# Kernel optimization log

Measured on AMD Instinct MI355X. Metric: run time of the kernel, lower is better.

Reference implementation:

```python
import jax, jax.numpy as jnp
import numpy as np

B, TQ, TK, D = 8, 2048, 2048, 1024


def setup_inputs() -> dict:
    key = jax.random.key(0)
    ks = jax.random.split(key, 9)
    s = 1.0 / np.sqrt(D)
    return {
        "query": jax.random.normal(ks[0], (B, TQ, D), jnp.float32),
        "keys": jax.random.normal(ks[1], (B, TK, D), jnp.float32),
        "Wq": jax.random.normal(ks[2], (D, D), jnp.float32) * s,
        "bq": jax.random.normal(ks[3], (D,), jnp.float32) * 0.01,
        "Wk": jax.random.normal(ks[4], (D, D), jnp.float32) * s,
        "bk": jax.random.normal(ks[5], (D,), jnp.float32) * 0.01,
        "Wv": jax.random.normal(ks[6], (D, D), jnp.float32) * s,
        "bv": jax.random.normal(ks[7], (D,), jnp.float32) * 0.01,
        "mask": jax.random.randint(ks[8], (B, TQ, TK), 0, 2, jnp.int32),
    }


def reference(query, keys, Wq, bq, Wk, bk, Wv, bv, mask):
    # Projections (torch Linear math; weights stored as [in, out])
    q = query @ Wq + bq            # [B, TQ, D]
    k = keys @ Wk + bk             # [B, TK, D]
    v = keys @ Wv + bv             # proj_values=True -> [B, TK, D]
    scale = 1.0 / jnp.sqrt(jnp.asarray(D, q.dtype))
    scores = jnp.einsum("bqd,bkd->bqk", q, k) * scale  # [B, TQ, TK]
    scores = jnp.where(mask == 0, jnp.asarray(-1e9, scores.dtype), scores)
    alphas = jax.nn.softmax(scores, axis=-1)
    context = jnp.einsum("bqk,bkd->bqd", alphas, v)    # [B, TQ, D]
    return context
```

## Files before the change

kernel.cpp:

```cpp
#include <hip/hip_runtime.h>
#include <hip/hip_bf16.h>

#define BB 8
#define TQn 2048
#define TKn 2048
#define DDn 1024

typedef float f32x4 __attribute__((ext_vector_type(4)));
typedef short bf16x8 __attribute__((ext_vector_type(8)));

__device__ __forceinline__ void async16(const void* g, void* l) {
    __builtin_amdgcn_global_load_lds(
        (const __attribute__((address_space(1))) void*)g,
        (__attribute__((address_space(3))) void*)l, 16, 0, 0);
}

__global__ __launch_bounds__(256) void prep_k(
    float* __restrict__ rowsum, float* __restrict__ biasqk,
    const float* __restrict__ bq, const float* __restrict__ bk) {
    int i = blockIdx.x * 256 + threadIdx.x;
    if (i < BB * TQn) rowsum[i] = 0.0f;
    if (i < DDn) biasqk[i] = bq[i];
    else if (i < 2 * DDn) biasqk[i] = bk[i - DDn];
}

__global__ __launch_bounds__(256) void cast2_k(
    const float* __restrict__ q, const float* __restrict__ k,
    __hip_bfloat16* __restrict__ xq, __hip_bfloat16* __restrict__ xk, size_t n8) {
    const float* in = blockIdx.y ? k : q;
    __hip_bfloat16* out = blockIdx.y ? xk : xq;
    size_t i = (size_t)blockIdx.x * blockDim.x + threadIdx.x;
    size_t stride = (size_t)gridDim.x * blockDim.x;
    for (; i < n8; i += stride) {
        const float4* p = (const float4*)in + i * 2;
        float4 a = p[0], b = p[1];
        union { __hip_bfloat16 h[8]; int4 qd; } u;
        u.h[0] = __float2bfloat16(a.x); u.h[1] = __float2bfloat16(a.y);
        u.h[2] = __float2bfloat16(a.z); u.h[3] = __float2bfloat16(a.w);
        u.h[4] = __float2bfloat16(b.x); u.h[5] = __float2bfloat16(b.y);
        u.h[6] = __float2bfloat16(b.z); u.h[7] = __float2bfloat16(b.w);
        ((int4*)out)[i] = u.qd;
    }
}

__global__ __launch_bounds__(256) void transpose3_k(
    const float* __restrict__ Wq, const float* __restrict__ Wk,
    const float* __restrict__ Wv, __hip_bfloat16* __restrict__ oq,
    __hip_bfloat16* __restrict__ ok, __hip_bfloat16* __restrict__ ov) {
    const float* in = blockIdx.z == 0 ? Wq : (blockIdx.z == 1 ? Wk : Wv);
    __hip_bfloat16* out = blockIdx.z == 0 ? oq : (blockIdx.z == 1 ? ok : ov);
    __shared__ float tile[32][33];
    int c0 = blockIdx.x * 32, r0 = blockIdx.y * 32;
    int tx = threadIdx.x, ty = threadIdx.y;
    #pragma unroll
    for (int i = 0; i < 32; i += 8)
        tile[ty + i][tx] = in[(size_t)(r0 + ty + i) * DDn + c0 + tx];
    __syncthreads();
    #pragma unroll
    for (int i = 0; i < 32; i += 8)
        out[(size_t)(c0 + ty + i) * DDn + r0 + tx] = __float2bfloat16(tile[tx][ty + i]);
}

#define M_PROJ_QK 0
#define M_PROJ_V  1
#define M_SCORES  2
#define M_CTX     3

#define STG(Pg, Psl, U, T, H) do { \
    const __hip_bfloat16* _g = Pg + (size_t)(T) * 64 + (H) * 32; \
    char* _l = Psl + (U) * 16384 + w * 2048; \
    async16(_g, _l); \
    async16(_g + 16 * Kd, _l + 1024); \
} while (0)

#define PHASE(U, S, STAGE_STMT, WAIT_STMT) do { \
    if ((S) == 0) { \
        _Pragma("unroll") \
        for (int m = 0; m < 8; m++) \
            af[m] = *(const bf16x8*)(Asl + (U) * 16384 + a_off + m * 1024); \
    } \
    bf[0] = *(const bf16x8*)(Bsl + (U) * 16384 + b_off + (S) * 2048); \
    bf[1] = *(const bf16x8*)(Bsl + (U) * 16384 + b_off + (S) * 2048 + 1024); \
    STAGE_STMT; \
    WAIT_STMT; \
    __builtin_amdgcn_sched_barrier(0); \
    __builtin_amdgcn_s_barrier(); \
    __builtin_amdgcn_s_setprio(1); \
    _Pragma("unroll") \
    for (int m = 0; m < 8; m++) { \
        acc[m][(S)*2]     = __builtin_amdgcn_mfma_f32_16x16x32_bf16(af[m], bf[0], acc[m][(S)*2], 0, 0, 0); \
        acc[m][(S)*2 + 1] = __builtin_amdgcn_mfma_f32_16x16x32_bf16(af[m], bf[1], acc[m][(S)*2 + 1], 0, 0, 0); \
    } \
    __builtin_amdgcn_s_setprio(0); \
    __builtin_amdgcn_sched_barrier(0); \
    __builtin_amdgcn_s_barrier(); \
} while (0)

template <int MODE>
__global__ __launch_bounds__(512, 2) void gemm256_k(
    const __hip_bfloat16* __restrict__ A, const __hip_bfloat16* __restrict__ B,
    void* __restrict__ Cout, const float* __restrict__ bias,
    const int* __restrict__ mask, float* __restrict__ rowsum,
    int K, long sA, long sB, long sC, float scale, int ldc) {
    __shared__ char smem[131072];
    char* Asl = smem;
    char* Bsl = smem + 65536;

    const int tid = threadIdx.x;
    const int lane = tid & 63;
    const int w = tid >> 6;
    const int wr = w >> 2, wc = w & 3;
    const int bn = blockIdx.x, bm = blockIdx.y, bz = blockIdx.z;
    const size_t Kd = (size_t)K;

    const int slog = (lane & 3) ^ ((lane >> 4) & 3);
    const __hip_bfloat16* Agl = A + (size_t)bz * sA
        + ((size_t)bm * 256 + 32 * w + (lane >> 2)) * Kd + slog * 8;
    const __hip_bfloat16* Bgl = B + (size_t)bz * sB
        + ((size_t)bn * 256 + 32 * w + (lane >> 2)) * Kd + slog * 8;

    const int sx16 = ((lane >> 4) ^ ((lane & 15) >> 2)) * 16;
    const int a_off = (wr * 128 + (lane & 15)) * 64 + sx16;
    const int b_off = (wc * 64 + (lane & 15)) * 64 + sx16;

    f32x4 acc[8][4] = {};
    bf16x8 af[8], bf[2];

    const int NI = K >> 7;

    STG(Agl, Asl, 0, 0, 0); STG(Bgl, Bsl, 0, 0, 0);
    STG(Agl, Asl, 1, 0, 1); STG(Bgl, Bsl, 1, 0, 1);
    STG(Agl, Asl, 2, 1, 0); STG(Bgl, Bsl, 2, 1, 0);
    asm volatile("s_waitcnt vmcnt(4)" ::: "memory");
    __builtin_amdgcn_sched_barrier(0);
    __builtin_amdgcn_s_barrier();

    for (int i = 0; i < NI; ++i) {
        const bool nx = (i + 1 < NI);
        const int t1 = 2 * i + 1, t2 = 2 * i + 2, t3 = 2 * i + 3;
        PHASE(0, 0, STG(Agl, Asl, 3, t1, 1), );
        PHASE(0, 1, STG(Bgl, Bsl, 3, t1, 1), );
        PHASE(1, 0, if (nx) STG(Agl, Asl, 0, t2, 0), );
        PHASE(1, 1, if (nx) STG(Bgl, Bsl, 0, t2, 0),
              if (nx) { asm volatile("s_waitcnt vmcnt(4)" ::: "memory"); }
              else    { asm volatile("s_waitcnt vmcnt(0)" ::: "memory"); });
        PHASE(2, 0, if (nx) STG(Agl, Asl, 1, t2, 1), );
        PHASE(2, 1, if (nx) STG(Bgl, Bsl, 1, t2, 1), );
        PHASE(3, 0, if (nx) STG(Agl, Asl, 2, t3, 0), );
        PHASE(3, 1, if (nx) STG(Bgl, Bsl, 2, t3, 0),
              if (nx) { asm volatile("s_waitcnt vmcnt(4)" ::: "memory"); });
    }

    const int rq = (lane >> 4) << 2;
    const int cl = lane & 15;

    if (MODE == M_SCORES) {
        const size_t mbase = (size_t)bz * ((size_t)TQn * TKn);
        #pragma unroll
        for (int m = 0; m < 8; m++) {
            const int grow0 = bm * 256 + wr * 128 + m * 16 + rq;
            float rs[4] = {0.0f, 0.0f, 0.0f, 0.0f};
            #pragma unroll
            for (int n = 0; n < 4; n++) {
                const int gcol = bn * 256 + wc * 64 + n * 16 + cl;
                #pragma unroll
                for (int r = 0; r < 4; r++) {
                    float v = acc[m][n][r] * scale;
                    int mk = mask[mbase + (size_t)(grow0 + r) * TKn + gcol];
                    float p = mk ? __expf(v) : 0.0f;
                    ((__hip_bfloat16*)Cout)[(size_t)bz * sC +
                        (size_t)(grow0 + r) * ldc + gcol] = __float2bfloat16(p);
                    rs[r] += p;
                }
            }
            #pragma unroll
            for (int off = 1; off < 16; off <<= 1) {
                #pragma unroll
                for (int r = 0; r < 4; r++) rs[r] += __shfl_xor(rs[r], off);
            }
            if (cl == 0) {
                float* rp = rowsum + bz * TQn + grow0;
                #pragma unroll
                for (int r = 0; r < 4; r++) atomicAdd(rp + r, rs[r]);
            }
        }
    } else if (MODE == M_CTX) {
        #pragma unroll
        for (int m = 0; m < 8; m++) {
            const int grow0 = bm * 256 + wr * 128 + m * 16 + rq;
            float inv[4];
            #pragma unroll
            for (int r = 0; r < 4; r++)
                inv[r] = 1.0f / rowsum[bz * TQn + grow0 + r];
            #pragma unroll
            for (int n = 0; n < 4; n++) {
                const int gcol = bn * 256 + wc * 64 + n * 16 + cl;
                #pragma unroll
                for (int r = 0; r < 4; r++)
                    ((float*)Cout)[(size_t)bz * sC + (size_t)(grow0 + r) * ldc + gcol] =
                        acc[m][n][r] * inv[r];
            }
        }
    } else {
        #pragma unroll
        for (int m = 0; m < 8; m++) {
            #pragma unroll
            for (int n = 0; n < 4; n++) {
                const int grow0 = bm * 256 + wr * 128 + m * 16 + rq;
                const int gcol = bn * 256 + wc * 64 + n * 16 + cl;
                float bv = (MODE == M_PROJ_QK) ? bias[bz * DDn + gcol] : 0.0f;
                #pragma unroll
                for (int r = 0; r < 4; r++) {
                    float v = acc[m][n][r] * scale +
                              ((MODE == M_PROJ_V) ? bias[grow0 + r] : bv);
                    ((__hip_bfloat16*)Cout)[(size_t)bz * sC +
                        (size_t)(grow0 + r) * ldc + gcol] = __float2bfloat16(v);
                }
            }
        }
    }
}

extern "C" void kernel_launch(void* const* d_in, const int* in_sizes, int n_in,
                              void* d_out, int out_size, void* d_ws, size_t ws_size,
                              hipStream_t stream) {
    const float* query = (const float*)d_in[0];
    const float* keys  = (const float*)d_in[1];
    const float* Wq = (const float*)d_in[2];
    const float* bq = (const float*)d_in[3];
    const float* Wk = (const float*)d_in[4];
    const float* bk = (const float*)d_in[5];
    const float* Wv = (const float*)d_in[6];
    const float* bv = (const float*)d_in[7];
    const int* mask = (const int*)d_in[8];
    float* out = (float*)d_out;

    char* ws = (char*)d_ws;
    const size_t NQ = (size_t)BB * TQn * DDn;
    __hip_bfloat16* xq_bf = (__hip_bfloat16*)(ws);
    __hip_bfloat16* xk_bf = (__hip_bfloat16*)(ws + 33554432);
    __hip_bfloat16* qb    = (__hip_bfloat16*)(ws + 67108864);
    __hip_bfloat16* kb    = (__hip_bfloat16*)(ws + 100663296);
    __hip_bfloat16* vtb   = (__hip_bfloat16*)(ws + 134217728);
    __hip_bfloat16* wq_t  = (__hip_bfloat16*)(ws + 167772160);
    __hip_bfloat16* wk_t  = (__hip_bfloat16*)(ws + 169869312);
    __hip_bfloat16* wv_t  = (__hip_bfloat16*)(ws + 171966464);
    float*          biasqk= (float*)         (ws + 174063616);
    float*          rowsum= (float*)         (ws + 174071808);
    __hip_bfloat16* P     = (__hip_bfloat16*)(ws);

    const float scale = 0.03125f;

    prep_k<<<64, 256, 0, stream>>>(rowsum, biasqk, bq, bk);
    cast2_k<<<dim3(1024, 2), 256, 0, stream>>>(query, keys, xq_bf, xk_bf, NQ / 8);
    transpose3_k<<<dim3(32, 32, 3), dim3(32, 8), 0, stream>>>(
        Wq, Wk, Wv, wq_t, wk_t, wv_t);
    gemm256_k<M_PROJ_QK><<<dim3(4, 64, 2), 512, 0, stream>>>(
        xq_bf, wq_t, qb, biasqk, nullptr, nullptr,
        DDn, 16777216L, 1048576L, 16777216L, 1.0f, DDn);
    gemm256_k<M_PROJ_V><<<dim3(8, 4, BB), 512, 0, stream>>>(
        wv_t, xk_bf, vtb, bv, nullptr, nullptr,
        DDn, 0, (long)TKn * DDn, (long)DDn * TKn, 1.0f, TKn);
    gemm256_k<M_SCORES><<<dim3(8, 8, BB), 512, 0, stream>>>(
        qb, kb, P, nullptr, mask, rowsum,
        DDn, (long)TQn * DDn, (long)TKn * DDn, (long)TQn * TKn, scale, TKn);
    gemm256_k<M_CTX><<<dim3(4, 8, BB), 512, 0, stream>>>(
        P, vtb, out, nullptr, nullptr, rowsum,
        TKn, (long)TQn * TKn, (long)DDn * TKn, (long)TQn * DDn, 1.0f, DDn);
}
```

Baseline: 572.6 us.

## Pack mask to bitmask and merge GEMM half-phases into single-barrier phases

```diff
diff --git a/kernel.cpp b/kernel.cpp
--- a/kernel.cpp
+++ b/kernel.cpp
@@ -15,13 +15,24 @@
         (__attribute__((address_space(3))) void*)l, 16, 0, 0);
 }
 
-__global__ __launch_bounds__(256) void prep_k(
+__global__ __launch_bounds__(256) void pack_mask_k(
+    const int* __restrict__ mask, unsigned long long* __restrict__ mask64,
     float* __restrict__ rowsum, float* __restrict__ biasqk,
     const float* __restrict__ bq, const float* __restrict__ bk) {
-    int i = blockIdx.x * 256 + threadIdx.x;
-    if (i < BB * TQn) rowsum[i] = 0.0f;
-    if (i < DDn) biasqk[i] = bq[i];
-    else if (i < 2 * DDn) biasqk[i] = bk[i - DDn];
+    const int bid = blockIdx.x, tid = threadIdx.x;
+    if (bid < 64) {
+        int i = bid * 256 + tid;
+        rowsum[i] = 0.0f;
+        if (i < DDn) biasqk[i] = bq[i];
+        else if (i < 2 * DDn) biasqk[i] = bk[i - DDn];
+    }
+    const int lane = tid & 63, wv = tid >> 6;
+    const int NW = BB * TQn * (TKn / 64);
+    for (int wd = bid * 4 + wv; wd < NW; wd += gridDim.x * 4) {
+        int m = mask[(size_t)wd * 64 + lane];
+        unsigned long long bits = __ballot(m != 0);
+        if (lane == 0) mask64[wd] = bits;
+    }
 }
 
 __global__ __launch_bounds__(256) void cast2_k(
@@ -73,14 +84,15 @@
     async16(_g + 16 * Kd, _l + 1024); \
 } while (0)
 
-#define PHASE(U, S, STAGE_STMT, WAIT_STMT) do { \
-    if ((S) == 0) { \
-        _Pragma("unroll") \
-        for (int m = 0; m < 8; m++) \
-            af[m] = *(const bf16x8*)(Asl + (U) * 16384 + a_off + m * 1024); \
-    } \
-    bf[0] = *(const bf16x8*)(Bsl + (U) * 16384 + b_off + (S) * 2048); \
-    bf[1] = *(const bf16x8*)(Bsl + (U) * 16384 + b_off + (S) * 2048 + 1024); \
+#define STG2(U, T, H) do { STG(Agl, Asl, U, T, H); STG(Bgl, Bsl, U, T, H); } while (0)
+
+#define PH4(U, STAGE_STMT, WAIT_STMT) do { \
+    _Pragma("unroll") \
+    for (int m = 0; m < 8; m++) \
+        af[m] = *(const bf16x8*)(Asl + (U) * 16384 + a_off + m * 1024); \
+    _Pragma("unroll") \
+    for (int j = 0; j < 4; j++) \
+        bf4[j] = *(const bf16x8*)(Bsl + (U) * 16384 + b_off + j * 1024); \
     STAGE_STMT; \
     WAIT_STMT; \
     __builtin_amdgcn_sched_barrier(0); \
@@ -88,19 +100,19 @@
     __builtin_amdgcn_s_setprio(1); \
     _Pragma("unroll") \
     for (int m = 0; m < 8; m++) { \
-        acc[m][(S)*2]     = __builtin_amdgcn_mfma_f32_16x16x32_bf16(af[m], bf[0], acc[m][(S)*2], 0, 0, 0); \
-        acc[m][(S)*2 + 1] = __builtin_amdgcn_mfma_f32_16x16x32_bf16(af[m], bf[1], acc[m][(S)*2 + 1], 0, 0, 0); \
+        _Pragma("unroll") \
+        for (int j = 0; j < 4; j++) \
+            acc[m][j] = __builtin_amdgcn_mfma_f32_16x16x32_bf16(af[m], bf4[j], acc[m][j], 0, 0, 0); \
     } \
     __builtin_amdgcn_s_setprio(0); \
     __builtin_amdgcn_sched_barrier(0); \
-    __builtin_amdgcn_s_barrier(); \
 } while (0)
 
 template <int MODE>
 __global__ __launch_bounds__(512, 2) void gemm256_k(
     const __hip_bfloat16* __restrict__ A, const __hip_bfloat16* __restrict__ B,
     void* __restrict__ Cout, const float* __restrict__ bias,
-    const int* __restrict__ mask, float* __restrict__ rowsum,
+    const unsigned long long* __restrict__ mask64, float* __restrict__ rowsum,
     int K, long sA, long sB, long sC, float scale, int ldc) {
     __shared__ char smem[131072];
     char* Asl = smem;
@@ -124,50 +136,51 @@
     const int b_off = (wc * 64 + (lane & 15)) * 64 + sx16;
 
     f32x4 acc[8][4] = {};
-    bf16x8 af[8], bf[2];
+    bf16x8 af[8], bf4[4];
 
     const int NI = K >> 7;
 
-    STG(Agl, Asl, 0, 0, 0); STG(Bgl, Bsl, 0, 0, 0);
-    STG(Agl, Asl, 1, 0, 1); STG(Bgl, Bsl, 1, 0, 1);
-    STG(Agl, Asl, 2, 1, 0); STG(Bgl, Bsl, 2, 1, 0);
-    asm volatile("s_waitcnt vmcnt(4)" ::: "memory");
+    STG2(0, 0, 0);
+    STG2(1, 0, 1);
+    STG2(2, 1, 0);
+    asm volatile("s_waitcnt vmcnt(8)" ::: "memory");
     __builtin_amdgcn_sched_barrier(0);
     __builtin_amdgcn_s_barrier();
 
     for (int i = 0; i < NI; ++i) {
         const bool nx = (i + 1 < NI);
-        const int t1 = 2 * i + 1, t2 = 2 * i + 2, t3 = 2 * i + 3;
-        PHASE(0, 0, STG(Agl, Asl, 3, t1, 1), );
-        PHASE(0, 1, STG(Bgl, Bsl, 3, t1, 1), );
-        PHASE(1, 0, if (nx) STG(Agl, Asl, 0, t2, 0), );
-        PHASE(1, 1, if (nx) STG(Bgl, Bsl, 0, t2, 0),
-              if (nx) { asm volatile("s_waitcnt vmcnt(4)" ::: "memory"); }
-              else    { asm volatile("s_waitcnt vmcnt(0)" ::: "memory"); });
-        PHASE(2, 0, if (nx) STG(Agl, Asl, 1, t2, 1), );
-        PHASE(2, 1, if (nx) STG(Bgl, Bsl, 1, t2, 1), );
-        PHASE(3, 0, if (nx) STG(Agl, Asl, 2, t3, 0), );
-        PHASE(3, 1, if (nx) STG(Bgl, Bsl, 2, t3, 0),
-              if (nx) { asm volatile("s_waitcnt vmcnt(4)" ::: "memory"); });
+        PH4(0, STG2(3, 2 * i + 1, 1),
+            asm volatile("s_waitcnt vmcnt(8)" ::: "memory"));
+        PH4(1, if (nx) STG2(0, 2 * i + 2, 0),
+            if (nx) { asm volatile("s_waitcnt vmcnt(8)" ::: "memory"); }
+            else    { asm volatile("s_waitcnt vmcnt(4)" ::: "memory"); });
+        PH4(2, if (nx) STG2(1, 2 * i + 2, 1),
+            if (nx) { asm volatile("s_waitcnt vmcnt(8)" ::: "memory"); }
+            else    { asm volatile("s_waitcnt vmcnt(0)" ::: "memory"); });
+        PH4(3, if (nx) STG2(2, 2 * i + 3, 0),
+            if (nx) { asm volatile("s_waitcnt vmcnt(8)" ::: "memory"); });
     }
 
     const int rq = (lane >> 4) << 2;
     const int cl = lane & 15;
 
     if (MODE == M_SCORES) {
-        const size_t mbase = (size_t)bz * ((size_t)TQn * TKn);
         #pragma unroll
         for (int m = 0; m < 8; m++) {
             const int grow0 = bm * 256 + wr * 128 + m * 16 + rq;
             float rs[4] = {0.0f, 0.0f, 0.0f, 0.0f};
+            unsigned long long mw[4];
+            #pragma unroll
+            for (int r = 0; r < 4; r++)
+                mw[r] = mask64[((size_t)bz * TQn + grow0 + r) * (TKn / 64)
+                               + (bn * 4 + wc)];
             #pragma unroll
             for (int n = 0; n < 4; n++) {
                 const int gcol = bn * 256 + wc * 64 + n * 16 + cl;
                 #pragma unroll
                 for (int r = 0; r < 4; r++) {
-                    float v = acc[m][n][r] * scale;
-                    int mk = mask[mbase + (size_t)(grow0 + r) * TKn + gcol];
-                    float p = mk ? __expf(v) : 0.0f;
+                    float p = ((mw[r] >> (n * 16 + cl)) & 1ULL)
+                                  ? __expf(acc[m][n][r] * scale) : 0.0f;
                     ((__hip_bfloat16*)Cout)[(size_t)bz * sC +
                         (size_t)(grow0 + r) * ldc + gcol] = __float2bfloat16(p);
                     rs[r] += p;
@@ -247,11 +260,12 @@
     __hip_bfloat16* wv_t  = (__hip_bfloat16*)(ws + 171966464);
     float*          biasqk= (float*)         (ws + 174063616);
     float*          rowsum= (float*)         (ws + 174071808);
+    unsigned long long* mask64 = (unsigned long long*)(ws + 174137344);
     __hip_bfloat16* P     = (__hip_bfloat16*)(ws);
 
     const float scale = 0.03125f;
 
-    prep_k<<<64, 256, 0, stream>>>(rowsum, biasqk, bq, bk);
+    pack_mask_k<<<2048, 256, 0, stream>>>(mask, mask64, rowsum, biasqk, bq, bk);
     cast2_k<<<dim3(1024, 2), 256, 0, stream>>>(query, keys, xq_bf, xk_bf, NQ / 8);
     transpose3_k<<<dim3(32, 32, 3), dim3(32, 8), 0, stream>>>(
         Wq, Wk, Wv, wq_t, wk_t, wv_t);
@@ -262,7 +276,7 @@
         wv_t, xk_bf, vtb, bv, nullptr, nullptr,
         DDn, 0, (long)TKn * DDn, (long)DDn * TKn, 1.0f, TKn);
     gemm256_k<M_SCORES><<<dim3(8, 8, BB), 512, 0, stream>>>(
-        qb, kb, P, nullptr, mask, rowsum,
+        qb, kb, P, nullptr, mask64, rowsum,
         DDn, (long)TQn * DDn, (long)TKn * DDn, (long)TQn * TKn, scale, TKn);
     gemm256_k<M_CTX><<<dim3(4, 8, BB), 512, 0, stream>>>(
         P, vtb, out, nullptr, nullptr, rowsum,
```

Result: slower. 595.4 us (+4.0%).
